# Performance work log

Measured on AMD Instinct MI355X. Metric: run time of the kernel, lower is better.

## Reference

```python
import jax, jax.numpy as jnp
import numpy as np

N_NODES = 100000
N_EDGES = 1600000
IN_DIM, HID_DIM, OUT_DIM = 128, 64, 40


def setup_inputs() -> dict:
    key = jax.random.key(0)
    k1, k2, k3, k4, k5, k6 = jax.random.split(key, 6)
    x = jax.random.normal(k1, (N_NODES, IN_DIM), dtype=jnp.float32)
    edge_index = jax.random.randint(k2, (2, N_EDGES), 0, N_NODES, dtype=jnp.int64)
    W1 = jax.random.normal(k3, (IN_DIM, HID_DIM), dtype=jnp.float32) * 0.05
    b1 = jnp.zeros((HID_DIM,), dtype=jnp.float32)
    W2 = jax.random.normal(k4, (HID_DIM, OUT_DIM), dtype=jnp.float32) * 0.05
    b2 = jnp.zeros((OUT_DIM,), dtype=jnp.float32)
    return {"x": x, "edge_index": edge_index, "W1": W1, "b1": b1, "W2": W2, "b2": b2}


def gcn_conv(x, src, dst, W, b, n_nodes):
    """PyG GCNConv: linear -> symmetric-normalized aggregation (with self loops) -> + bias."""
    h = x @ W                                                # [N, C_out]
    # degree of targets, including the implicit self loop (weight 1 each)
    deg = jax.ops.segment_sum(jnp.ones_like(dst, dtype=h.dtype), dst,
                              num_segments=n_nodes) + 1.0    # [N]
    dinv = jax.lax.rsqrt(deg)                                # deg >= 1, always valid
    norm = dinv[src] * dinv[dst]                             # [E] edge norm coefficients
    msg = h[src] * norm[:, None]                             # [E, C_out] gather + scale
    agg = jax.ops.segment_sum(msg, dst, num_segments=n_nodes)
    # self-loop contribution: norm_ii = dinv_i * dinv_i
    agg = agg + h * (dinv * dinv)[:, None]
    return agg + b


def reference(x, edge_index, W1, b1, W2, b2):
    src, dst = edge_index[0], edge_index[1]  # source_to_target flow (PyG default)
    n = x.shape[0]
    h = gcn_conv(x, src, dst, W1, b1, n)
    h = jax.nn.relu(h)
    # dropout is identity in eval mode (training=False)
    out = gcn_conv(h, src, dst, W2, b2, n)
    return out
```

## Files before the change

kernel.cpp:

```cpp
#include <hip/hip_runtime.h>
#include <math.h>

#define N_NODES 100000
#define N_EDGES 1600000
#define IN_DIM 128
#define HID_DIM 64
#define OUT_DIM 40

#define NPAD 102400

#define BUCKET_SHIFT 7
#define BUCKET_NODES 128
#define N_BUCKETS 782
#define CHUNK 8192
#define N_CHUNKS 200

typedef _Float16 f16;
typedef _Float16 f16x4 __attribute__((ext_vector_type(4)));
typedef _Float16 f16x8 __attribute__((ext_vector_type(8)));
typedef float f32x4 __attribute__((ext_vector_type(4)));


__global__ __launch_bounds__(1024) void hist_kernel(const int* __restrict__ dst,
                                                    int* __restrict__ hist,
                                                    const float* __restrict__ W1,
                                                    const float* __restrict__ W2,
                                                    f16* __restrict__ w1f,
                                                    f16* __restrict__ w2f) {
    __shared__ int lh[N_BUCKETS];
    int c = blockIdx.x;
    int t = threadIdx.x;
    if (c < N_CHUNKS) {
        for (int b = t; b < N_BUCKETS; b += 1024) lh[b] = 0;
        __syncthreads();
        const int4* d4 = (const int4*)dst;
        int i0 = c * (CHUNK / 4);
#pragma unroll
        for (int r = 0; r < 2; ++r) {
            int idx = i0 + r * 1024 + t;
            if (idx < N_EDGES / 4) {
                int4 d = d4[idx];
                atomicAdd(&lh[d.x >> BUCKET_SHIFT], 1);
                atomicAdd(&lh[d.y >> BUCKET_SHIFT], 1);
                atomicAdd(&lh[d.z >> BUCKET_SHIFT], 1);
                atomicAdd(&lh[d.w >> BUCKET_SHIFT], 1);
            }
        }
        __syncthreads();
        for (int b = t; b < N_BUCKETS; b += 1024) hist[b * N_CHUNKS + c] = lh[b];
    } else if (c == N_CHUNKS) {
        if (t < 1024) {
            int g = t;
            int f = g >> 6, L = g & 63;
            int s = f >> 2, cc = f & 3;
            int q = L >> 4, n = L & 15;
            f16x8 v;
#pragma unroll
            for (int j = 0; j < 8; ++j)
                v[j] = (f16)W1[(32 * s + 8 * q + j) * HID_DIM + 16 * cc + n];
            *(f16x8*)&w1f[(size_t)g * 8] = v;
        }
    } else {
        if (t < 384) {
            int g = t;
            int f = g >> 6, L = g & 63;
            int s = f / 3, cc = f % 3;
            int q = L >> 4, n = L & 15;
            int col = 16 * cc + n;
            f16x8 v;
#pragma unroll
            for (int j = 0; j < 8; ++j)
                v[j] = (col < OUT_DIM) ? (f16)W2[(32 * s + 8 * q + j) * OUT_DIM + col] : (f16)0.f;
            *(f16x8*)&w2f[(size_t)g * 8] = v;
        }
    }
}

__global__ __launch_bounds__(256) void scan_chunks_kernel(const int* __restrict__ hist,
                                                          int* __restrict__ base,
                                                          int* __restrict__ bucketTotal) {
    __shared__ int lds[256];
    int b = blockIdx.x;
    int t = threadIdx.x;
    int cv = (t < N_CHUNKS) ? hist[b * N_CHUNKS + t] : 0;
    lds[t] = cv;
    __syncthreads();
    for (int off = 1; off < 256; off <<= 1) {
        int val = (t >= off) ? lds[t - off] : 0;
        __syncthreads();
        lds[t] += val;
        __syncthreads();
    }
    if (t < N_CHUNKS) base[b * N_CHUNKS + t] = lds[t] - cv;
    if (t == 255) bucketTotal[b] = lds[255];
}

__global__ __launch_bounds__(256) void scan_buckets_kernel(const int* __restrict__ bucketTotal,
                                                           int* __restrict__ bucketBase) {
    __shared__ int lds[256];
    int t = threadIdx.x;
    int v[4];
    int s = 0;
    for (int k = 0; k < 4; ++k) {
        int b = 4 * t + k;
        int cv = (b < N_BUCKETS) ? bucketTotal[b] : 0;
        v[k] = s;
        s += cv;
    }
    lds[t] = s;
    __syncthreads();
    for (int off = 1; off < 256; off <<= 1) {
        int val = (t >= off) ? lds[t - off] : 0;
        __syncthreads();
        lds[t] += val;
        __syncthreads();
    }
    int excl = (t == 0) ? 0 : lds[t - 1];
    for (int k = 0; k < 4; ++k) {
        int b = 4 * t + k;
        if (b < N_BUCKETS) bucketBase[b] = excl + v[k];
    }
}

__global__ __launch_bounds__(1024) void scatter_kernel(const int* __restrict__ src,
                                                       const int* __restrict__ dst,
                                                       const int* __restrict__ base,
                                                       const int* __restrict__ bucketBase,
                                                       int* __restrict__ stage) {
    __shared__ int lbase[N_BUCKETS];
    __shared__ int lcnt[N_BUCKETS];
    int bid = blockIdx.x;
    int chunk = (bid & 7) * 25 + (bid >> 3);
    int t = threadIdx.x;
    for (int b = t; b < N_BUCKETS; b += 1024) {
        lbase[b] = base[b * N_CHUNKS + chunk] + bucketBase[b];
        lcnt[b] = 0;
    }
    __syncthreads();
    const int4* s4 = (const int4*)src;
    const int4* d4 = (const int4*)dst;
    int i0 = chunk * (CHUNK / 4);
#pragma unroll
    for (int r = 0; r < 2; ++r) {
        int idx = i0 + r * 1024 + t;
        if (idx < N_EDGES / 4) {
            int4 sv = s4[idx];
            int4 dv = d4[idx];
            int d, b, pos;
            d = dv.x; b = d >> BUCKET_SHIFT;
            pos = lbase[b] + atomicAdd(&lcnt[b], 1);
            stage[pos] = ((d & (BUCKET_NODES - 1)) << 17) | sv.x;
            d = dv.y; b = d >> BUCKET_SHIFT;
            pos = lbase[b] + atomicAdd(&lcnt[b], 1);
            stage[pos] = ((d & (BUCKET_NODES - 1)) << 17) | sv.y;
            d = dv.z; b = d >> BUCKET_SHIFT;
            pos = lbase[b] + atomicAdd(&lcnt[b], 1);
            stage[pos] = ((d & (BUCKET_NODES - 1)) << 17) | sv.z;
            d = dv.w; b = d >> BUCKET_SHIFT;
            pos = lbase[b] + atomicAdd(&lcnt[b], 1);
            stage[pos] = ((d & (BUCKET_NODES - 1)) << 17) | sv.w;
        }
    }
}

__global__ __launch_bounds__(256) void place_kernel(const int* __restrict__ stage,
                                                    const int* __restrict__ bucketBase,
                                                    int* __restrict__ csr,
                                                    int* __restrict__ row_start,
                                                    int* __restrict__ cnt,
                                                    float* __restrict__ dinv) {
    __shared__ int lhist[BUCKET_NODES];
    __shared__ int lscan[BUCKET_NODES];
    __shared__ int lstart[BUCKET_NODES];
    __shared__ int lcur[BUCKET_NODES];
    int b = blockIdx.x;
    int t = threadIdx.x;
    int est = bucketBase[b];
    int een = (b == N_BUCKETS - 1) ? N_EDGES : bucketBase[b + 1];
    if (t < BUCKET_NODES) { lhist[t] = 0; lcur[t] = 0; }
    __syncthreads();
    for (int e = est + t; e < een; e += 256) atomicAdd(&lhist[stage[e] >> 17], 1);
    __syncthreads();
    if (t < BUCKET_NODES) lscan[t] = lhist[t];
    __syncthreads();
    for (int off = 1; off < BUCKET_NODES; off <<= 1) {
        int val = (t >= off && t < BUCKET_NODES) ? lscan[t - off] : 0;
        __syncthreads();
        if (t < BUCKET_NODES) lscan[t] += val;
        __syncthreads();
    }
    if (t < BUCKET_NODES) {
        int myexcl = (t == 0) ? 0 : lscan[t - 1];
        lstart[t] = est + myexcl;
        int node = (b << BUCKET_SHIFT) + t;
        if (node < N_NODES) {
            row_start[node] = est + myexcl;
            cnt[node] = lhist[t];
            dinv[node] = rsqrtf((float)lhist[t] + 1.0f);
        }
    }
    __syncthreads();
    for (int e = est + t; e < een; e += 256) {
        int rec = stage[e];
        int dl = rec >> 17;
        int pos = lstart[dl] + atomicAdd(&lcur[dl], 1);
        csr[pos] = rec & 0x1FFFF;
    }
}

__global__ __launch_bounds__(256) void gemm1_kernel(const float* __restrict__ x,
                                                    const f16* __restrict__ w1f,
                                                    const float* __restrict__ dinv,
                                                    f16* __restrict__ h1p) {
    __shared__ f16 aT[1088 * 8];
    int t = threadIdx.x;
    int nodeBase = blockIdx.x * 64;
    int L = t & 63;

    const f16x8* w1f8 = (const f16x8*)w1f;
    f16x8 bfrag[16];
#pragma unroll
    for (int f = 0; f < 16; ++f) bfrag[f] = w1f8[f * 64 + L];

#pragma unroll
    for (int i = 0; i < 8; ++i) {
        int idx = i * 256 + t;
        int node = idx >> 5;
        int col4 = idx & 31;
        int gnode = nodeBase + node;
        if (gnode >= N_NODES) gnode = N_NODES - 1;
        float4 v = *(const float4*)&x[(size_t)gnode * IN_DIM + col4 * 4];
        int w = node >> 4, m = node & 15;
        int s = col4 >> 3, q = (col4 >> 1) & 3, j0 = (col4 & 1) * 4;
        f16x4 h;
        h.x = (f16)v.x; h.y = (f16)v.y; h.z = (f16)v.z; h.w = (f16)v.w;
        int idx16 = (w * 4 + s) * 68 + 17 * q + m;
        *(f16x4*)&aT[idx16 * 8 + j0] = h;
    }
    __syncthreads();

    int wv = t >> 6;
    int q = L >> 4, m = L & 15;
    f32x4 acc[4] = {};
#pragma unroll
    for (int s = 0; s < 4; ++s) {
        f16x8 afrag = *(const f16x8*)&aT[((wv * 4 + s) * 68 + 17 * q + m) * 8];
#pragma unroll
        for (int c = 0; c < 4; ++c)
            acc[c] = __builtin_amdgcn_mfma_f32_16x16x32_f16(afrag, bfrag[s * 4 + c], acc[c], 0, 0, 0);
    }

#pragma unroll
    for (int r = 0; r < 4; ++r) {
        int node = nodeBase + 16 * wv + q * 4 + r;
        if (node < N_NODES) {
            float di = dinv[node];
#pragma unroll
            for (int c = 0; c < 4; ++c)
                h1p[(size_t)node * HID_DIM + 16 * c + m] = (f16)(acc[c][r] * di);
        }
    }
}

#define ZSTR 72
#define H2STR 64
__global__ __launch_bounds__(256) void agg1mm_kernel(const f16* __restrict__ h1p,
                                                     const int* __restrict__ csr,
                                                     const int* __restrict__ row_start,
                                                     const int* __restrict__ cnt,
                                                     const float* __restrict__ dinv,
                                                     const float* __restrict__ b1,
                                                     const f16* __restrict__ w2f,
                                                     f16* __restrict__ h2p) {
    __shared__ f16 zT[64 * ZSTR];
    int t = threadIdx.x;
    int nodeBase = blockIdx.x * 64;
    int wv = t >> 6;
    int L = t & 63;
    int g = L >> 3;
    int s = L & 7;
    const f16x8* h8 = (const f16x8*)h1p;
    float bb[8];
#pragma unroll
    for (int j = 0; j < 8; ++j) bb[j] = b1[8 * s + j];

    for (int p = 0; p < 2; ++p) {
        int nodeLocal = 16 * wv + 8 * p + g;
        int node = nodeBase + nodeLocal;
        float acc[8];
#pragma unroll
        for (int j = 0; j < 8; ++j) acc[j] = 0.f;
        int lim = 0;
        const int* cp = csr;
        bool valid = (node < N_NODES);
        if (valid) {
            f16x8 sv = h8[(size_t)node * 8 + s];
#pragma unroll
            for (int j = 0; j < 8; ++j) acc[j] = (float)sv[j];
            lim = cnt[node];
            cp = csr + row_start[node];
        }
        for (int k = 0; k < lim; k += 8) {
            int ii[8]; float mm[8];
#pragma unroll
            for (int u = 0; u < 8; ++u) {
                int kk = k + u;
                bool ok = (kk < lim);
                ii[u] = cp[ok ? kk : k];
                mm[u] = ok ? 1.f : 0.f;
            }
            f16x8 f[8];
#pragma unroll
            for (int u = 0; u < 8; ++u) f[u] = h8[(size_t)ii[u] * 8 + s];
#pragma unroll
            for (int j = 0; j < 8; ++j) {
                float t0 = 0.f;
#pragma unroll
                for (int u = 0; u < 8; ++u) t0 += mm[u] * (float)f[u][j];
                acc[j] += t0;
            }
        }
        f16x8 o;
        if (valid) {
            float di = dinv[node];
#pragma unroll
            for (int j = 0; j < 8; ++j) {
                float v = acc[j] * di + bb[j];
                o[j] = (f16)(v > 0.f ? v : 0.f);
            }
        } else {
#pragma unroll
            for (int j = 0; j < 8; ++j) o[j] = (f16)0.f;
        }
        *(f16x8*)&zT[nodeLocal * ZSTR + 8 * s] = o;
    }
    __syncthreads();

    int q = L >> 4, m = L & 15;
    const f16x8* w2f8 = (const f16x8*)w2f;
    f32x4 acc2[3] = {};
#pragma unroll
    for (int ks = 0; ks < 2; ++ks) {
        f16x8 afrag = *(const f16x8*)&zT[(16 * wv + m) * ZSTR + 32 * ks + 8 * q];
#pragma unroll
        for (int c = 0; c < 3; ++c)
            acc2[c] = __builtin_amdgcn_mfma_f32_16x16x32_f16(afrag, w2f8[(ks * 3 + c) * 64 + L], acc2[c], 0, 0, 0);
    }
#pragma unroll
    for (int r = 0; r < 4; ++r) {
        int node = nodeBase + 16 * wv + q * 4 + r;
        if (node < N_NODES) {
            float di = dinv[node];
            h2p[(size_t)node * H2STR + m]      = (f16)(acc2[0][r] * di);
            h2p[(size_t)node * H2STR + 16 + m] = (f16)(acc2[1][r] * di);
            if (m < 8)
                h2p[(size_t)node * H2STR + 32 + m] = (f16)(acc2[2][r] * di);
        }
    }
}

__global__ __launch_bounds__(256) void agg2_kernel(const f16* __restrict__ h2p,
                                                   const int* __restrict__ csr,
                                                   const int* __restrict__ row_start,
                                                   const int* __restrict__ cnt,
                                                   const float* __restrict__ dinv,
                                                   const float* __restrict__ b2,
                                                   float* __restrict__ out) {
    int t = threadIdx.x;
    int L = t & 63;
    int wv = t >> 6;
    int g = (L * 13) >> 6;
    int s = L - 5 * g;
    int node = blockIdx.x * 48 + wv * 12 + g;
    if (g >= 12 || node >= N_NODES) return;
    const f16x8* h8 = (const f16x8*)h2p;
    float acc[8];
    {
        f16x8 sv = h8[(size_t)node * 8 + s];
#pragma unroll
        for (int j = 0; j < 8; ++j) acc[j] = (float)sv[j];
    }
    int lim = cnt[node];
    const int* cp = csr + row_start[node];
    for (int k = 0; k < lim; k += 8) {
        int ii[8]; float mm[8];
#pragma unroll
        for (int u = 0; u < 8; ++u) {
            int kk = k + u;
            bool ok = (kk < lim);
            ii[u] = cp[ok ? kk : k];
            mm[u] = ok ? 1.f : 0.f;
        }
        f16x8 f[8];
#pragma unroll
        for (int u = 0; u < 8; ++u) f[u] = h8[(size_t)ii[u] * 8 + s];
#pragma unroll
        for (int j = 0; j < 8; ++j) {
            float t0 = 0.f;
#pragma unroll
            for (int u = 0; u < 8; ++u) t0 += mm[u] * (float)f[u][j];
            acc[j] += t0;
        }
    }
    float di = dinv[node];
    float4 o0, o1;
    o0.x = acc[0] * di + b2[8 * s + 0];
    o0.y = acc[1] * di + b2[8 * s + 1];
    o0.z = acc[2] * di + b2[8 * s + 2];
    o0.w = acc[3] * di + b2[8 * s + 3];
    o1.x = acc[4] * di + b2[8 * s + 4];
    o1.y = acc[5] * di + b2[8 * s + 5];
    o1.z = acc[6] * di + b2[8 * s + 6];
    o1.w = acc[7] * di + b2[8 * s + 7];
    *(float4*)&out[(size_t)node * OUT_DIM + 8 * s] = o0;
    *(float4*)&out[(size_t)node * OUT_DIM + 8 * s + 4] = o1;
}

extern "C" void kernel_launch(void* const* d_in, const int* in_sizes, int n_in,
                              void* d_out, int out_size, void* d_ws, size_t ws_size,
                              hipStream_t stream) {
    const float* x  = (const float*)d_in[0];
    const int*   ei = (const int*)d_in[1];
    const float* W1 = (const float*)d_in[2];
    const float* b1 = (const float*)d_in[3];
    const float* W2 = (const float*)d_in[4];
    const float* b2 = (const float*)d_in[5];
    float* out = (float*)d_out;

    const int* src = ei;
    const int* dst = ei + N_EDGES;

    int* wsi        = (int*)d_ws;
    int* hist       = wsi;
    int* base       = hist + N_BUCKETS * N_CHUNKS;
    int* bucketTotal= base + N_BUCKETS * N_CHUNKS;
    int* bucketBase = bucketTotal + 1024;
    int* row_start  = bucketBase + 1024;
    int* cnt        = row_start + NPAD;
    int* csr        = cnt + NPAD;
    int* stage      = csr + N_EDGES;
    float* dinv     = (float*)(stage + N_EDGES);
    f16*   h1p      = (f16*)(dinv + NPAD);
    f16*   h2p      = h1p + (size_t)N_NODES * HID_DIM;
    f16*   w1f      = h2p + (size_t)N_NODES * H2STR;
    f16*   w2f      = w1f + 8192;

    hist_kernel<<<N_CHUNKS + 2, 1024, 0, stream>>>(dst, hist, W1, W2, w1f, w2f);
    scan_chunks_kernel<<<N_BUCKETS, 256, 0, stream>>>(hist, base, bucketTotal);
    scan_buckets_kernel<<<1, 256, 0, stream>>>(bucketTotal, bucketBase);
    scatter_kernel<<<N_CHUNKS, 1024, 0, stream>>>(src, dst, base, bucketBase, stage);
    place_kernel<<<N_BUCKETS, 256, 0, stream>>>(stage, bucketBase, csr, row_start, cnt, dinv);
    gemm1_kernel<<<(N_NODES + 63) / 64, 256, 0, stream>>>(x, w1f, dinv, h1p);
    agg1mm_kernel<<<(N_NODES + 63) / 64, 256, 0, stream>>>(h1p, csr, row_start, cnt, dinv, b1, w2f, h2p);
    agg2_kernel<<<(N_NODES + 47) / 48, 256, 0, stream>>>(h2p, csr, row_start, cnt, dinv, b2, out);
}
```

Baseline: 198.6 us.

## Stage CSR neighbor lists in LDS, fuse bucket scan, drop cnt array

```diff
diff --git a/kernel.cpp b/kernel.cpp
--- a/kernel.cpp
+++ b/kernel.cpp
@@ -15,6 +15,9 @@
 #define CHUNK 8192
 #define N_CHUNKS 200
 
+#define CSR_CAP1 2048
+#define CSR_CAP2 1280
+
 typedef _Float16 f16;
 typedef _Float16 f16x4 __attribute__((ext_vector_type(4)));
 typedef _Float16 f16x8 __attribute__((ext_vector_type(8)));
@@ -26,7 +29,8 @@
                                                     const float* __restrict__ W1,
                                                     const float* __restrict__ W2,
                                                     f16* __restrict__ w1f,
-                                                    f16* __restrict__ w2f) {
+                                                    f16* __restrict__ w2f,
+                                                    int* __restrict__ done) {
     __shared__ int lh[N_BUCKETS];
     int c = blockIdx.x;
     int t = threadIdx.x;
@@ -49,7 +53,8 @@
         __syncthreads();
         for (int b = t; b < N_BUCKETS; b += 1024) hist[b * N_CHUNKS + c] = lh[b];
     } else if (c == N_CHUNKS) {
-        if (t < 1024) {
+        if (t == 0) *done = 0;
+        {
             int g = t;
             int f = g >> 6, L = g & 63;
             int s = f >> 2, cc = f & 3;
@@ -78,8 +83,11 @@
 
 __global__ __launch_bounds__(256) void scan_chunks_kernel(const int* __restrict__ hist,
                                                           int* __restrict__ base,
-                                                          int* __restrict__ bucketTotal) {
+                                                          int* __restrict__ bucketTotal,
+                                                          int* __restrict__ bucketBase,
+                                                          int* __restrict__ done) {
     __shared__ int lds[256];
+    __shared__ int isLast;
     int b = blockIdx.x;
     int t = threadIdx.x;
     int cv = (t < N_CHUNKS) ? hist[b * N_CHUNKS + t] : 0;
@@ -93,32 +101,36 @@
     }
     if (t < N_CHUNKS) base[b * N_CHUNKS + t] = lds[t] - cv;
     if (t == 255) bucketTotal[b] = lds[255];
-}
-
-__global__ __launch_bounds__(256) void scan_buckets_kernel(const int* __restrict__ bucketTotal,
-                                                           int* __restrict__ bucketBase) {
-    __shared__ int lds[256];
-    int t = threadIdx.x;
-    int v[4];
-    int s = 0;
-    for (int k = 0; k < 4; ++k) {
-        int b = 4 * t + k;
-        int cv = (b < N_BUCKETS) ? bucketTotal[b] : 0;
-        v[k] = s;
-        s += cv;
-    }
-    lds[t] = s;
-    __syncthreads();
-    for (int off = 1; off < 256; off <<= 1) {
-        int val = (t >= off) ? lds[t - off] : 0;
-        __syncthreads();
-        lds[t] += val;
-        __syncthreads();
-    }
-    int excl = (t == 0) ? 0 : lds[t - 1];
-    for (int k = 0; k < 4; ++k) {
-        int b = 4 * t + k;
-        if (b < N_BUCKETS) bucketBase[b] = excl + v[k];
+    __syncthreads();
+    if (t == 0) {
+        __threadfence();
+        int prev = atomicAdd(done, 1);
+        isLast = (prev == N_BUCKETS - 1) ? 1 : 0;
+    }
+    __syncthreads();
+    if (isLast) {
+        __threadfence();
+        int v[4];
+        int s = 0;
+        for (int k = 0; k < 4; ++k) {
+            int bb = 4 * t + k;
+            int c2 = (bb < N_BUCKETS) ? bucketTotal[bb] : 0;
+            v[k] = s;
+            s += c2;
+        }
+        lds[t] = s;
+        __syncthreads();
+        for (int off = 1; off < 256; off <<= 1) {
+            int val = (t >= off) ? lds[t - off] : 0;
+            __syncthreads();
+            lds[t] += val;
+            __syncthreads();
+        }
+        int excl = (t == 0) ? 0 : lds[t - 1];
+        for (int k = 0; k < 4; ++k) {
+            int bb = 4 * t + k;
+            if (bb < N_BUCKETS) bucketBase[bb] = excl + v[k];
+        }
     }
 }
 
@@ -167,7 +179,6 @@
                                                     const int* __restrict__ bucketBase,
                                                     int* __restrict__ csr,
                                                     int* __restrict__ row_start,
-                                                    int* __restrict__ cnt,
                                                     float* __restrict__ dinv) {
     __shared__ int lhist[BUCKET_NODES];
     __shared__ int lscan[BUCKET_NODES];
@@ -193,11 +204,8 @@
         int myexcl = (t == 0) ? 0 : lscan[t - 1];
         lstart[t] = est + myexcl;
         int node = (b << BUCKET_SHIFT) + t;
-        if (node < N_NODES) {
-            row_start[node] = est + myexcl;
-            cnt[node] = lhist[t];
-            dinv[node] = rsqrtf((float)lhist[t] + 1.0f);
-        }
+        if (node <= N_NODES) row_start[node] = est + myexcl;
+        if (node < N_NODES) dinv[node] = rsqrtf((float)lhist[t] + 1.0f);
     }
     __syncthreads();
     for (int e = est + t; e < een; e += 256) {
@@ -267,18 +275,33 @@
 __global__ __launch_bounds__(256) void agg1mm_kernel(const f16* __restrict__ h1p,
                                                      const int* __restrict__ csr,
                                                      const int* __restrict__ row_start,
-                                                     const int* __restrict__ cnt,
                                                      const float* __restrict__ dinv,
                                                      const float* __restrict__ b1,
                                                      const f16* __restrict__ w2f,
                                                      f16* __restrict__ h2p) {
     __shared__ f16 zT[64 * ZSTR];
+    __shared__ int lrs[65];
+    __shared__ int lcsr[CSR_CAP1];
     int t = threadIdx.x;
     int nodeBase = blockIdx.x * 64;
     int wv = t >> 6;
     int L = t & 63;
     int g = L >> 3;
     int s = L & 7;
+
+    if (t < 65) {
+        int gi = nodeBase + t;
+        lrs[t] = row_start[(gi <= N_NODES) ? gi : N_NODES];
+    }
+    __syncthreads();
+    int rs0 = lrs[0];
+    int seg = lrs[64] - rs0;
+    bool staged = (seg <= CSR_CAP1);
+    if (staged) {
+        for (int i = t; i < seg; i += 256) lcsr[i] = csr[rs0 + i];
+    }
+    __syncthreads();
+
     const f16x8* h8 = (const f16x8*)h1p;
     float bb[8];
 #pragma unroll
@@ -287,39 +310,41 @@
     for (int p = 0; p < 2; ++p) {
         int nodeLocal = 16 * wv + 8 * p + g;
         int node = nodeBase + nodeLocal;
+        bool valid = (node < N_NODES);
+        int rs = lrs[nodeLocal];
+        int lim = lrs[nodeLocal + 1] - rs;
         float acc[8];
 #pragma unroll
         for (int j = 0; j < 8; ++j) acc[j] = 0.f;
-        int lim = 0;
-        const int* cp = csr;
-        bool valid = (node < N_NODES);
         if (valid) {
             f16x8 sv = h8[(size_t)node * 8 + s];
 #pragma unroll
             for (int j = 0; j < 8; ++j) acc[j] = (float)sv[j];
-            lim = cnt[node];
-            cp = csr + row_start[node];
-        }
-        for (int k = 0; k < lim; k += 8) {
-            int ii[8]; float mm[8];
-#pragma unroll
-            for (int u = 0; u < 8; ++u) {
-                int kk = k + u;
-                bool ok = (kk < lim);
-                ii[u] = cp[ok ? kk : k];
-                mm[u] = ok ? 1.f : 0.f;
+        }
+        auto gather = [&](const auto* cp) {
+            for (int k = 0; k < lim; k += 8) {
+                int ii[8]; float mm[8];
+#pragma unroll
+                for (int u = 0; u < 8; ++u) {
+                    int kk = k + u;
+                    bool ok = (kk < lim);
+                    ii[u] = cp[ok ? kk : k];
+                    mm[u] = ok ? 1.f : 0.f;
+                }
+                f16x8 f[8];
+#pragma unroll
+                for (int u = 0; u < 8; ++u) f[u] = h8[(size_t)ii[u] * 8 + s];
+#pragma unroll
+                for (int j = 0; j < 8; ++j) {
+                    float t0 = 0.f;
+#pragma unroll
+                    for (int u = 0; u < 8; ++u) t0 += mm[u] * (float)f[u][j];
+                    acc[j] += t0;
+                }
             }
-            f16x8 f[8];
-#pragma unroll
-            for (int u = 0; u < 8; ++u) f[u] = h8[(size_t)ii[u] * 8 + s];
-#pragma unroll
-            for (int j = 0; j < 8; ++j) {
-                float t0 = 0.f;
-#pragma unroll
-                for (int u = 0; u < 8; ++u) t0 += mm[u] * (float)f[u][j];
-                acc[j] += t0;
-            }
-        }
+        };
+        if (staged) gather(lcsr + (rs - rs0));
+        else        gather(csr + rs);
         f16x8 o;
         if (valid) {
             float di = dinv[node];
@@ -362,46 +387,66 @@
 __global__ __launch_bounds__(256) void agg2_kernel(const f16* __restrict__ h2p,
                                                    const int* __restrict__ csr,
                                                    const int* __restrict__ row_start,
-                                                   const int* __restrict__ cnt,
                                                    const float* __restrict__ dinv,
                                                    const float* __restrict__ b2,
                                                    float* __restrict__ out) {
-    int t = threadIdx.x;
+    __shared__ int lrs[49];
+    __shared__ int lcsr[CSR_CAP2];
+    int t = threadIdx.x;
+    int nodeBase = blockIdx.x * 48;
+    if (t < 49) {
+        int gi = nodeBase + t;
+        lrs[t] = row_start[(gi <= N_NODES) ? gi : N_NODES];
+    }
+    __syncthreads();
+    int rs0 = lrs[0];
+    int seg = lrs[48] - rs0;
+    bool staged = (seg <= CSR_CAP2);
+    if (staged) {
+        for (int i = t; i < seg; i += 256) lcsr[i] = csr[rs0 + i];
+    }
+    __syncthreads();
+
     int L = t & 63;
     int wv = t >> 6;
     int g = (L * 13) >> 6;
     int s = L - 5 * g;
-    int node = blockIdx.x * 48 + wv * 12 + g;
+    int nodeLocal = wv * 12 + g;
+    int node = nodeBase + nodeLocal;
     if (g >= 12 || node >= N_NODES) return;
     const f16x8* h8 = (const f16x8*)h2p;
+    int rs = lrs[nodeLocal];
+    int lim = lrs[nodeLocal + 1] - rs;
     float acc[8];
     {
         f16x8 sv = h8[(size_t)node * 8 + s];
 #pragma unroll
         for (int j = 0; j < 8; ++j) acc[j] = (float)sv[j];
     }
-    int lim = cnt[node];
-    const int* cp = csr + row_start[node];
-    for (int k = 0; k < lim; k += 8) {
-        int ii[8]; float mm[8];
-#pragma unroll
-        for (int u = 0; u < 8; ++u) {
-            int kk = k + u;
-            bool ok = (kk < lim);
-            ii[u] = cp[ok ? kk : k];
-            mm[u] = ok ? 1.f : 0.f;
-        }
-        f16x8 f[8];
-#pragma unroll
-        for (int u = 0; u < 8; ++u) f[u] = h8[(size_t)ii[u] * 8 + s];
-#pragma unroll
-        for (int j = 0; j < 8; ++j) {
-            float t0 = 0.f;
-#pragma unroll
-            for (int u = 0; u < 8; ++u) t0 += mm[u] * (float)f[u][j];
-            acc[j] += t0;
-        }
-    }
+    auto gather = [&](const auto* cp) {
+        for (int k = 0; k < lim; k += 8) {
+            int ii[8]; float mm[8];
+#pragma unroll
+            for (int u = 0; u < 8; ++u) {
+                int kk = k + u;
+                bool ok = (kk < lim);
+                ii[u] = cp[ok ? kk : k];
+                mm[u] = ok ? 1.f : 0.f;
+            }
+            f16x8 f[8];
+#pragma unroll
+            for (int u = 0; u < 8; ++u) f[u] = h8[(size_t)ii[u] * 8 + s];
+#pragma unroll
+            for (int j = 0; j < 8; ++j) {
+                float t0 = 0.f;
+#pragma unroll
+                for (int u = 0; u < 8; ++u) t0 += mm[u] * (float)f[u][j];
+                acc[j] += t0;
+            }
+        }
+    };
+    if (staged) gather(lcsr + (rs - rs0));
+    else        gather(csr + rs);
     float di = dinv[node];
     float4 o0, o1;
     o0.x = acc[0] * di + b2[8 * s + 0];
@@ -435,9 +480,9 @@
     int* base       = hist + N_BUCKETS * N_CHUNKS;
     int* bucketTotal= base + N_BUCKETS * N_CHUNKS;
     int* bucketBase = bucketTotal + 1024;
-    int* row_start  = bucketBase + 1024;
-    int* cnt        = row_start + NPAD;
-    int* csr        = cnt + NPAD;
+    int* done       = bucketBase + 1024;
+    int* row_start  = done + 1024;
+    int* csr        = row_start + NPAD;
     int* stage      = csr + N_EDGES;
     float* dinv     = (float*)(stage + N_EDGES);
     f16*   h1p      = (f16*)(dinv + NPAD);
@@ -445,12 +490,11 @@
     f16*   w1f      = h2p + (size_t)N_NODES * H2STR;
     f16*   w2f      = w1f + 8192;
 
-    hist_kernel<<<N_CHUNKS + 2, 1024, 0, stream>>>(dst, hist, W1, W2, w1f, w2f);
-    scan_chunks_kernel<<<N_BUCKETS, 256, 0, stream>>>(hist, base, bucketTotal);
-    scan_buckets_kernel<<<1, 256, 0, stream>>>(bucketTotal, bucketBase);
+    hist_kernel<<<N_CHUNKS + 2, 1024, 0, stream>>>(dst, hist, W1, W2, w1f, w2f, done);
+    scan_chunks_kernel<<<N_BUCKETS, 256, 0, stream>>>(hist, base, bucketTotal, bucketBase, done);
     scatter_kernel<<<N_CHUNKS, 1024, 0, stream>>>(src, dst, base, bucketBase, stage);
-    place_kernel<<<N_BUCKETS, 256, 0, stream>>>(stage, bucketBase, csr, row_start, cnt, dinv);
+    place_kernel<<<N_BUCKETS, 256, 0, stream>>>(stage, bucketBase, csr, row_start, dinv);
     gemm1_kernel<<<(N_NODES + 63) / 64, 256, 0, stream>>>(x, w1f, dinv, h1p);
-    agg1mm_kernel<<<(N_NODES + 63) / 64, 256, 0, stream>>>(h1p, csr, row_start, cnt, dinv, b1, w2f, h2p);
-    agg2_kernel<<<(N_NODES + 47) / 48, 256, 0, stream>>>(h2p, csr, row_start, cnt, dinv, b2, out);
-}
+    agg1mm_kernel<<<(N_NODES + 63) / 64, 256, 0, stream>>>(h1p, csr, row_start, dinv, b1, w2f, h2p);
+    agg2_kernel<<<(N_NODES + 47) / 48, 256, 0, stream>>>(h2p, csr, row_start, dinv, b2, out);
+}
```

Result: slower. 215.0 us (+8.3%).
